# Kernel optimization log

Hardware: AMD Instinct MI355X
Metric: run time of the kernel (lower is better)

Reference implementation:

```python
import jax, jax.numpy as jnp
import numpy as np
from jax import lax

V, D, B, L, T, H, C = 100000, 128, 512, 20, 20, 32, 33
N, E = B * L, B * (L - 1)
SCALE = 12.0

def _l2n(x, eps=1e-12):
    return x / (jnp.linalg.norm(x, axis=-1, keepdims=True) + eps)

def setup_inputs():
    key = jax.random.key(0)
    ks = jax.random.split(key, 30)
    stdv = 1.0 / np.sqrt(D)
    u = lambda k, s: jax.random.uniform(k, s, jnp.float32, -stdv, stdv)
    params = dict(
        emb=u(ks[0], (V, D)),
        W1=u(ks[1], (D, D)), W2=u(ks[2], (D, D)),
        gru_wih=u(ks[3], (3 * D, 2 * D)), gru_whh=u(ks[4], (3 * D, D)),
        gru_bih=u(ks[5], (3 * D,)), gru_bhh=u(ks[6], (3 * D,)),
        fcu_w=u(ks[7], (D, D)), fcv_w=u(ks[8], (D, D)), fcv_b=u(ks[9], (D,)),
        fce_w=u(ks[10], (D,)), fcsr_w=u(ks[11], (D, 2 * D)),
        red_w=u(ks[12], (H, D)), red_b=u(ks[13], (H,)),
        rec_w=u(ks[14], (D, H)), rec_b=u(ks[15], (D,)),
        cde_w1=u(ks[16], (128, H)), cde_b1=u(ks[17], (128,)),
        cde_w2=u(ks[18], (C * H, 128)), cde_b2=u(ks[19], (C * H,)),
        init_w=u(ks[20], (H, C)), init_b=u(ks[21], (H,)),
    )
    nodes = jnp.arange(N).reshape(B, L)  # B session graphs, L nodes each
    params.update(
        w=jax.random.uniform(ks[22], (E,), jnp.float32, 0.1, 1.0),
        times=jnp.cumsum(jax.random.uniform(ks[23], (B, T), jnp.float32, 0.05, 1.0), axis=1),
        iid=jax.random.randint(ks[24], (N,), 0, V),
        src=nodes[:, :-1].reshape(-1),
        dst=nodes[:, 1:].reshape(-1),
        seg_ids=jnp.repeat(jnp.arange(B), L),
        last_nodes=nodes[:, -1],
        embeds_ids=jax.random.randint(ks[25], (B, T), 0, V),
    )
    return params

def reference(emb, W1, W2, gru_wih, gru_whh, gru_bih, gru_bhh, fcu_w, fcv_w, fcv_b,
              fce_w, fcsr_w, red_w, red_b, rec_w, rec_b, cde_w1, cde_b1, cde_w2,
              cde_b2, init_w, init_b, w, times, iid, src, dst, seg_ids, last_nodes,
              embeds_ids):
    feat = _l2n(emb[iid])  # [N,D]
    # --- SRGNN layer: edge-weighted mean message passing (both directions) + GRUCell ---
    def wmean(s, d):
        msum = jax.ops.segment_sum(feat[s] * w[:, None], d, num_segments=N)
        wsum = jax.ops.segment_sum(w, d, num_segments=N)[:, None]
        return jnp.where(wsum > 0, msum / jnp.where(wsum == 0, 1.0, wsum), 0.0)
    hn = jnp.concatenate([wmean(src, dst) @ W1.T, wmean(dst, src) @ W2.T], axis=1)
    gi = hn @ gru_wih.T + gru_bih
    gh = feat @ gru_whh.T + gru_bhh
    i_r, i_z, i_n = jnp.split(gi, 3, axis=1)
    h_r, h_z, h_n = jnp.split(gh, 3, axis=1)
    r = jax.nn.sigmoid(i_r + h_r)
    zg = jax.nn.sigmoid(i_z + h_z)
    ng = jnp.tanh(i_n + r * h_n)
    out = (1.0 - zg) * ng + zg * feat  # NOTE: computed but unused downstream, exactly as original
    # --- neural CDE over the session item sequence (linear interp knots at t=0..T-1, RK4 per knot) ---
    fode = _l2n(emb[embeds_ids] @ red_w.T + red_b)          # [B,T,H]
    X = jnp.concatenate([times[..., None], fode], axis=-1)  # [B,T,C]
    z0 = X[:, 0] @ init_w.T + init_b                        # [B,H]
    def fz(zt):
        h1 = jax.nn.relu(zt @ cde_w1.T + cde_b1)
        return jnp.tanh(h1 @ cde_w2.T + cde_b2).reshape(B, H, C)
    dX = jnp.swapaxes(X[:, 1:] - X[:, :-1], 0, 1)           # [T-1,B,C] piecewise-constant dX/dt
    def step(zt, dx):
        g = lambda zz: jnp.einsum('bhc,bc->bh', fz(zz), dx)
        k1 = g(zt); k2 = g(zt + 0.5 * k1); k3 = g(zt + 0.5 * k2); k4 = g(zt + k3)
        return zt + (k1 + 2.0 * k2 + 2.0 * k3 + k4) / 6.0, None
    zT, _ = lax.scan(step, z0, dX)
    time_embeds = zT @ rec_w.T + rec_b                      # [B,D]
    # --- attention readout over graph segments ---
    featn = feat / jnp.linalg.norm(feat, axis=-1, keepdims=True)  # no-eps renorm, as original
    fu = featn @ fcu_w.T
    fv = featn[last_nodes] @ fcv_w.T + fcv_b
    e = jax.nn.sigmoid(fu + fv[seg_ids]) @ fce_w            # [N]
    emax = jax.ops.segment_max(e, seg_ids, num_segments=B)
    ee = jnp.exp(e - emax[seg_ids])
    alpha = ee / jax.ops.segment_sum(ee, seg_ids, num_segments=B)[seg_ids]
    sr_g = jax.ops.segment_sum(featn * alpha[:, None], seg_ids, num_segments=B)
    sr_l = featn[last_nodes]
    sr = _l2n(jnp.concatenate([sr_l, sr_g], axis=1) @ fcsr_w.T + time_embeds)
    logits = sr @ _l2n(emb).T                               # [B,V]
    return jax.nn.log_softmax(SCALE * logits, axis=-1)
```

## Files before the change

kernel.cpp:

```cpp
#include <hip/hip_runtime.h>
#include <cstdint>

#define VN 100000
#define DD 128
#define BB 512
#define LL 20
#define TT 20
#define HH 32
#define CC 33
#define NC (HH*CC)

typedef unsigned int u32;

#define DEV static __device__ __forceinline__

DEV float tanh_fast(float x){ float e=__expf(2.f*x); return 1.f - 2.f/(e+1.f); }

DEV float rdlane(float v, int l){
  return __int_as_float(__builtin_amdgcn_readlane(__float_as_int(v), l));
}

__global__ __launch_bounds__(512, 2) void k_cde(
    const float* __restrict__ emb, const int* __restrict__ eids,
    const float* __restrict__ times,
    const float* __restrict__ red_w, const float* __restrict__ red_b,
    const float* __restrict__ w1, const float* __restrict__ b1,
    const float* __restrict__ w2, const float* __restrict__ b2,
    const float* __restrict__ iw, const float* __restrict__ ib,
    const float* __restrict__ rw, const float* __restrict__ rb,
    float* __restrict__ te){
  __shared__ float s_u[40*DD + 32*129];
  __shared__ float s_X[2*TT*CC];
  __shared__ float s_b1[DD];
  __shared__ float s_h1[2*DD];
  __shared__ float s_z[64], s_zs[64], s_ks[64], s_kp[64], s_kt[64];
  __shared__ float s_dx[2*CC];
  const int t = threadIdx.x;
  const int b0 = blockIdx.x*2;
  const int lane = t & 63;
  const int wv = t >> 6;
  const int h  = t >> 4;
  const int q  = t & 15;
  float* s_er = s_u;
  float* s_rw = s_u + 40*DD;
  float* s_w1 = s_u;

  float w2c[DD];
  {
    const float4* rc4 = (const float4*)(w2 + (size_t)(h*CC+q)*DD);
    #pragma unroll
    for (int j4=0;j4<32;j4++){
      float4 v = rc4[j4];
      w2c[4*j4]=v.x; w2c[4*j4+1]=v.y; w2c[4*j4+2]=v.z; w2c[4*j4+3]=v.w;
    }
  }
  const float b2c = b2[h*CC+q];
  const float b2s = b2[h*CC+16+q];
  const float* rs = w2 + (size_t)(h*CC+16+q)*DD;
  float w2t[8], b2t[4];
  #pragma unroll
  for (int r=0;r<4;r++){
    const float* tr = w2 + (size_t)((4*wv+r)*CC+32)*DD;
    w2t[2*r]   = tr[lane];
    w2t[2*r+1] = tr[64+lane];
    b2t[r]     = b2[(4*wv+r)*CC+32];
  }

  for (int i=t;i<HH*DD;i+=512){ int hh=i>>7, d=i&127; s_rw[hh*129+d]=red_w[i]; }
  if (t<40){ int g=t/TT, tt2=t%TT; s_X[(g*TT+tt2)*CC]=times[(b0+g)*TT+tt2]; }
  for (int pi=t;pi<40*DD;pi+=512){ int r=pi>>7, e=pi&127;
      s_er[pi]=emb[(size_t)eids[b0*TT+r]*DD+e]; }
  __syncthreads();
  for (int task=t; task<40*HH; task+=512){
    int r=task>>5, hh=task&31;
    const float* wr=s_rw+hh*129;
    const float* er=s_er+(size_t)r*DD;
    float acc=red_b[hh];
    #pragma unroll 16
    for(int e=0;e<DD;e++) acc += er[e]*wr[e];
    float ssq=acc*acc;
    #pragma unroll
    for(int o=16;o>0;o>>=1) ssq+=__shfl_xor(ssq,o,32);
    s_X[r*CC+1+hh]=acc/(sqrtf(ssq)+1e-12f);
  }
  __syncthreads();
  for (int i=t;i<DD*HH;i+=512){ int j=i>>5, hh=i&31; s_w1[j*33+hh]=w1[i]; }
  if (t<DD) s_b1[t]=b1[t];
  if (t<64){
    int g=t>>5, hh=t&31;
    float acc=ib[hh];
    const float* x0=s_X+(size_t)(g*TT)*CC;
    #pragma unroll
    for(int c=0;c<CC;c++) acc += x0[c]*iw[hh*CC+c];
    s_z[t]=acc; s_zs[t]=acc;
  }
  __syncthreads();

  const float4* rs4=(const float4*)rs;
  for (int step=0; step<TT-1; step++){
    if (t<2*CC){ int g=t/CC, c=t-g*CC;
      s_dx[t]=s_X[(g*TT+step+1)*CC+c]-s_X[(g*TT+step)*CC+c]; }
    for (int s=0;s<4;s++){
      float4 c0=rs4[0], c1=rs4[1], c2=rs4[2], c3=rs4[3];
      if (t<256){
        const int g=t>>7, j=t&127, gb=(t>>7)*32;
        float zsv=s_zs[lane];
        float acc=s_b1[j];
        const float* wj=s_w1+j*33;
        #pragma unroll
        for(int hh=0;hh<HH;hh++) acc += rdlane(zsv, gb+hh)*wj[hh];
        s_h1[g*DD+j]=fmaxf(acc,0.f);
      }
      __syncthreads();
      {
        float h00=s_h1[lane],    h01=s_h1[64+lane];
        float h10=s_h1[DD+lane], h11=s_h1[DD+64+lane];
        float a00=b2c, a01=b2c, a10=b2s, a11=b2s;
        #pragma unroll
        for (int jc=0;jc<8;jc++){
          float4 n0=c0,n1=c1,n2=c2,n3=c3;
          if (jc<7){ n0=rs4[4*jc+4]; n1=rs4[4*jc+5]; n2=rs4[4*jc+6]; n3=rs4[4*jc+7]; }
          float cf[16]={c0.x,c0.y,c0.z,c0.w, c1.x,c1.y,c1.z,c1.w,
                        c2.x,c2.y,c2.z,c2.w, c3.x,c3.y,c3.z,c3.w};
          #pragma unroll
          for (int jj=0;jj<16;jj++){
            const int j=jc*16+jj;
            float s0 = (j<64)? rdlane(h00,j) : rdlane(h01,j-64);
            float s1 = (j<64)? rdlane(h10,j) : rdlane(h11,j-64);
            a00 += s0*w2c[j]; a01 += s1*w2c[j];
            a10 += s0*cf[jj]; a11 += s1*cf[jj];
          }
          c0=n0; c1=n1; c2=n2; c3=n3;
        }
        float pk0 = tanh_fast(a00)*s_dx[q]    + tanh_fast(a10)*s_dx[16+q];
        float pk1 = tanh_fast(a01)*s_dx[CC+q] + tanh_fast(a11)*s_dx[CC+16+q];
        #pragma unroll
        for (int o=8;o>0;o>>=1){ pk0+=__shfl_xor(pk0,o,16); pk1+=__shfl_xor(pk1,o,16); }
        if (q==0){ s_kp[h]=pk0; s_kp[32+h]=pk1; }
        float p0=w2t[0]*h00+w2t[1]*h01;
        float p1=w2t[0]*h10+w2t[1]*h11;
        float p2=w2t[2]*h00+w2t[3]*h01;
        float p3=w2t[2]*h10+w2t[3]*h11;
        float p4=w2t[4]*h00+w2t[5]*h01;
        float p5=w2t[4]*h10+w2t[5]*h11;
        float p6=w2t[6]*h00+w2t[7]*h01;
        float p7=w2t[6]*h10+w2t[7]*h11;
        #pragma unroll
        for (int o=1;o<64;o<<=1){
          p0+=__shfl_xor(p0,o,64); p1+=__shfl_xor(p1,o,64);
          p2+=__shfl_xor(p2,o,64); p3+=__shfl_xor(p3,o,64);
          p4+=__shfl_xor(p4,o,64); p5+=__shfl_xor(p5,o,64);
          p6+=__shfl_xor(p6,o,64); p7+=__shfl_xor(p7,o,64);
        }
        if (lane==0){
          float dt0=s_dx[32], dt1=s_dx[CC+32];
          s_kt[4*wv+0]   =tanh_fast(p0+b2t[0])*dt0;
          s_kt[32+4*wv+0]=tanh_fast(p1+b2t[0])*dt1;
          s_kt[4*wv+1]   =tanh_fast(p2+b2t[1])*dt0;
          s_kt[32+4*wv+1]=tanh_fast(p3+b2t[1])*dt1;
          s_kt[4*wv+2]   =tanh_fast(p4+b2t[2])*dt0;
          s_kt[32+4*wv+2]=tanh_fast(p5+b2t[2])*dt1;
          s_kt[4*wv+3]   =tanh_fast(p6+b2t[3])*dt0;
          s_kt[32+4*wv+3]=tanh_fast(p7+b2t[3])*dt1;
        }
      }
      __syncthreads();
      if (t<64){
        float k=s_kp[t]+s_kt[t];
        float zv=s_z[t];
        if(s==0){ s_ks[t]=k;        s_zs[t]=zv+0.5f*k; }
        else if(s==1){ s_ks[t]+=2.f*k; s_zs[t]=zv+0.5f*k; }
        else if(s==2){ s_ks[t]+=2.f*k; s_zs[t]=zv+k; }
        else { float zn=zv+(s_ks[t]+k)*(1.f/6.f); s_z[t]=zn; s_zs[t]=zn; }
      }
      __syncthreads();
    }
  }
  if (t<256){
    const int g=t>>7, d=t&127;
    float acc=rb[d];
    const float* zz=s_z+g*HH;
    const float4* rv=(const float4*)(rw + (size_t)d*HH);
    #pragma unroll
    for(int jj=0;jj<8;jj++){
      float4 vv=rv[jj];
      acc += zz[4*jj]*vv.x + zz[4*jj+1]*vv.y + zz[4*jj+2]*vv.z + zz[4*jj+3]*vv.w;
    }
    te[(size_t)(b0+g)*DD+d]=acc;
  }
}

__global__ __launch_bounds__(128) void k_attn(
    const float* __restrict__ emb, const int* __restrict__ iid,
    const int* __restrict__ last_nodes,
    const float* __restrict__ fcu_w, const float* __restrict__ fcv_w,
    const float* __restrict__ fcv_b, const float* __restrict__ fce_w,
    const float* __restrict__ fcsr_w,
    const float* __restrict__ te, float* __restrict__ sr){
  __shared__ float s_fn[LL*DD];
  __shared__ float s_inv[LL];
  __shared__ float s_e[LL], s_alpha[LL], s_red[2], s_sg[DD], s_fl[DD];
  const int t=threadIdx.x, b=blockIdx.x;
  for(int p=t;p<LL*DD;p+=128){
    int r=p>>7, e=p&127;
    s_fn[p]=emb[(size_t)iid[b*LL+r]*DD+e];
  }
  __syncthreads();
  { int w=t>>6, lane=t&63;
    for(int r=w;r<LL;r+=2){
      float a=s_fn[r*DD+lane], c=s_fn[r*DD+lane+64];
      float s=a*a+c*c;
      #pragma unroll
      for(int o=32;o>0;o>>=1) s+=__shfl_xor(s,o,64);
      if(lane==0) s_inv[r]=1.f/sqrtf(s);
    }
  }
  __syncthreads();
  for(int p=t;p<LL*DD;p+=128) s_fn[p]*=s_inv[p>>7];
  __syncthreads();
  int lr=last_nodes[b]-b*LL; if(lr<0||lr>=LL) lr=LL-1;
  s_fl[t]=s_fn[lr*DD+t];
  __syncthreads();
  float fv;
  {
    float acc=fcv_b[t];
    const float* wv=fcv_w + t*DD;
    #pragma unroll 8
    for(int j=0;j<DD;j++) acc += s_fl[j]*wv[j];
    fv=acc;
  }
  const float fce=fce_w[t];
  const float* wu=fcu_w + t*DD;
  for(int n=0;n<LL;n++){
    float fu=0.f;
    #pragma unroll 8
    for(int j=0;j<DD;j++) fu += s_fn[n*DD+j]*wu[j];
    float sv = fce/(1.f+__expf(-(fu+fv)));
    #pragma unroll
    for(int o=32;o>0;o>>=1) sv += __shfl_xor(sv,o,64);
    if((t&63)==0) s_red[t>>6]=sv;
    __syncthreads();
    if(t==0) s_e[n]=s_red[0]+s_red[1];
    __syncthreads();
  }
  if(t<64){
    float ev=(t<LL)? s_e[t] : -1e30f;
    float m=ev;
    #pragma unroll
    for(int o=32;o>0;o>>=1) m=fmaxf(m,__shfl_xor(m,o,64));
    float ex=(t<LL)? __expf(ev-m):0.f;
    float ssum=ex;
    #pragma unroll
    for(int o=32;o>0;o>>=1) ssum+=__shfl_xor(ssum,o,64);
    if(t<LL) s_alpha[t]=ex/ssum;
  }
  __syncthreads();
  float sg=0.f;
  for(int n=0;n<LL;n++) sg += s_alpha[n]*s_fn[n*DD+t];
  s_sg[t]=sg;
  __syncthreads();
  float pre=te[(size_t)b*DD+t];
  const float* wsr=fcsr_w + t*2*DD;
  #pragma unroll 8
  for(int j=0;j<DD;j++) pre += s_fl[j]*wsr[j];
  #pragma unroll 8
  for(int j=0;j<DD;j++) pre += s_sg[j]*wsr[DD+j];
  float ss=pre*pre;
  #pragma unroll
  for(int o=32;o>0;o>>=1) ss+=__shfl_xor(ss,o,64);
  if((t&63)==0) s_red[t>>6]=ss;
  __syncthreads();
  float tot=s_red[0]+s_red[1];
  sr[(size_t)b*DD+t]=pre/(sqrtf(tot)+1e-12f);
}

__global__ __launch_bounds__(256, 2) void k_logits(
    const float* __restrict__ emb, const float* __restrict__ srr,
    float* __restrict__ out){
  const int v=blockIdx.x*256+threadIdx.x;
  if(v>=VN) return;
  const int bstart=blockIdx.y*256;
  float er[DD];
  {
    const float4* ev=(const float4*)emb + (size_t)v*32;
    #pragma unroll
    for(int j=0;j<32;j++){
      float4 u=ev[j];
      er[j*4+0]=u.x; er[j*4+1]=u.y; er[j*4+2]=u.z; er[j*4+3]=u.w;
    }
  }
  float nrm=0.f;
  #pragma unroll
  for(int d=0;d<DD;d++) nrm += er[d]*er[d];
  const float rn=12.f/(sqrtf(nrm)+1e-12f);
  for(int b=bstart;b<bstart+256;b++){
    const float* s=srr+(size_t)b*DD;
    float acc=0.f;
    #pragma unroll
    for(int d=0;d<DD;d++) acc += er[d]*s[d];
    out[(size_t)b*VN+v]=acc*rn;
  }
}

__global__ __launch_bounds__(256) void k_lse(const float* __restrict__ out,
                                             float* __restrict__ lse){
  const int b=blockIdx.x, t=threadIdx.x;
  const float4* rp=(const float4*)(out + (size_t)b*VN);
  float m=-1e30f, s=0.f;
  for(int i=t;i<VN/4;i+=256){
    float4 x=rp[i];
    float mx=fmaxf(fmaxf(x.x,x.y),fmaxf(x.z,x.w));
    if(mx>m){ s=s*__expf(m-mx); m=mx; }
    s += __expf(x.x-m)+__expf(x.y-m)+__expf(x.z-m)+__expf(x.w-m);
  }
  __shared__ float sm[256], ssb[256];
  sm[t]=m; ssb[t]=s;
  __syncthreads();
  for(int o=128;o>0;o>>=1){
    if(t<o){
      float m1=sm[t], m2=sm[t+o], s1=ssb[t], s2=ssb[t+o];
      float mm=fmaxf(m1,m2);
      sm[t]=mm; ssb[t]=s1*__expf(m1-mm)+s2*__expf(m2-mm);
    }
    __syncthreads();
  }
  if(t==0) lse[b]=sm[0]+logf(ssb[0]);
}

__global__ __launch_bounds__(256) void k_sub(float* __restrict__ out,
                                             const float* __restrict__ lse){
  const size_t i=(size_t)blockIdx.x*256+threadIdx.x;
  const int b=(int)((i*4)/VN);
  const float l=lse[b];
  float4* p=(float4*)out;
  float4 x=p[i];
  x.x-=l; x.y-=l; x.z-=l; x.w-=l;
  p[i]=x;
}

extern "C" void kernel_launch(void* const* d_in, const int* in_sizes, int n_in,
                              void* d_out, int out_size, void* d_ws, size_t ws_size,
                              hipStream_t stream){
  const float* emb    = (const float*)d_in[0];
  const float* fcu_w  = (const float*)d_in[7];
  const float* fcv_w  = (const float*)d_in[8];
  const float* fcv_b  = (const float*)d_in[9];
  const float* fce_w  = (const float*)d_in[10];
  const float* fcsr_w = (const float*)d_in[11];
  const float* red_w  = (const float*)d_in[12];
  const float* red_b  = (const float*)d_in[13];
  const float* rec_w  = (const float*)d_in[14];
  const float* rec_b  = (const float*)d_in[15];
  const float* cde_w1 = (const float*)d_in[16];
  const float* cde_b1 = (const float*)d_in[17];
  const float* cde_w2 = (const float*)d_in[18];
  const float* cde_b2 = (const float*)d_in[19];
  const float* init_w = (const float*)d_in[20];
  const float* init_b = (const float*)d_in[21];
  const float* times  = (const float*)d_in[23];
  const int* iid    = (const int*)d_in[24];
  const int* last_nodes = (const int*)d_in[28];
  const int* embeds_ids = (const int*)d_in[29];
  float* out = (float*)d_out;

  float* ws  = (float*)d_ws;
  float* te  = ws;
  float* sr  = te + (size_t)BB*DD;
  float* lse = sr + (size_t)BB*DD;

  k_cde   <<<BB/2, 512, 0, stream>>>(emb, embeds_ids, times, red_w, red_b,
                                     cde_w1, cde_b1, cde_w2, cde_b2,
                                     init_w, init_b, rec_w, rec_b, te);
  k_attn  <<<BB, 128, 0, stream>>>(emb, iid, last_nodes, fcu_w, fcv_w, fcv_b,
                                   fce_w, fcsr_w, te, sr);
  k_logits<<<dim3((VN+255)/256, 2), 256, 0, stream>>>(emb, sr, out);
  k_lse   <<<BB, 256, 0, stream>>>(out, lse);
  k_sub   <<<(int)(((size_t)BB*VN/4+255)/256), 256, 0, stream>>>(out, lse);
}
```

Before: 3.304 ms.

## Batch four sessions per CDE block and tile logits over staged session vectors

```diff
diff --git a/kernel.cpp b/kernel.cpp
--- a/kernel.cpp
+++ b/kernel.cpp
@@ -9,6 +9,7 @@
 #define HH 32
 #define CC 33
 #define NC (HH*CC)
+#define GG 4
 
 typedef unsigned int u32;
 
@@ -20,7 +21,7 @@
   return __int_as_float(__builtin_amdgcn_readlane(__float_as_int(v), l));
 }
 
-__global__ __launch_bounds__(512, 2) void k_cde(
+__global__ __launch_bounds__(512) void k_cde(
     const float* __restrict__ emb, const int* __restrict__ eids,
     const float* __restrict__ times,
     const float* __restrict__ red_w, const float* __restrict__ red_b,
@@ -29,49 +30,29 @@
     const float* __restrict__ iw, const float* __restrict__ ib,
     const float* __restrict__ rw, const float* __restrict__ rb,
     float* __restrict__ te){
-  __shared__ float s_u[40*DD + 32*129];
-  __shared__ float s_X[2*TT*CC];
+  __shared__ float s_u[GG*TT*DD + 32*129];
+  __shared__ float s_X[GG*TT*CC];
   __shared__ float s_b1[DD];
-  __shared__ float s_h1[2*DD];
-  __shared__ float s_z[64], s_zs[64], s_ks[64], s_kp[64], s_kt[64];
-  __shared__ float s_dx[2*CC];
+  __shared__ float s_b2[NC];
+  __shared__ float s_h1[GG*DD];
+  __shared__ float s_z[GG*HH], s_zs[GG*HH], s_ks[GG*HH], s_kp[GG*HH], s_kt[GG*HH];
+  __shared__ float s_dx[GG*CC];
   const int t = threadIdx.x;
-  const int b0 = blockIdx.x*2;
+  const int b0 = blockIdx.x*GG;
   const int lane = t & 63;
   const int wv = t >> 6;
   const int h  = t >> 4;
   const int q  = t & 15;
   float* s_er = s_u;
-  float* s_rw = s_u + 40*DD;
+  float* s_rw = s_u + GG*TT*DD;
   float* s_w1 = s_u;
 
-  float w2c[DD];
-  {
-    const float4* rc4 = (const float4*)(w2 + (size_t)(h*CC+q)*DD);
-    #pragma unroll
-    for (int j4=0;j4<32;j4++){
-      float4 v = rc4[j4];
-      w2c[4*j4]=v.x; w2c[4*j4+1]=v.y; w2c[4*j4+2]=v.z; w2c[4*j4+3]=v.w;
-    }
-  }
-  const float b2c = b2[h*CC+q];
-  const float b2s = b2[h*CC+16+q];
-  const float* rs = w2 + (size_t)(h*CC+16+q)*DD;
-  float w2t[8], b2t[4];
-  #pragma unroll
-  for (int r=0;r<4;r++){
-    const float* tr = w2 + (size_t)((4*wv+r)*CC+32)*DD;
-    w2t[2*r]   = tr[lane];
-    w2t[2*r+1] = tr[64+lane];
-    b2t[r]     = b2[(4*wv+r)*CC+32];
-  }
-
   for (int i=t;i<HH*DD;i+=512){ int hh=i>>7, d=i&127; s_rw[hh*129+d]=red_w[i]; }
-  if (t<40){ int g=t/TT, tt2=t%TT; s_X[(g*TT+tt2)*CC]=times[(b0+g)*TT+tt2]; }
-  for (int pi=t;pi<40*DD;pi+=512){ int r=pi>>7, e=pi&127;
+  if (t<GG*TT){ int g=t/TT, tt2=t%TT; s_X[(g*TT+tt2)*CC]=times[(b0+g)*TT+tt2]; }
+  for (int pi=t;pi<GG*TT*DD;pi+=512){ int r=pi>>7, e=pi&127;
       s_er[pi]=emb[(size_t)eids[b0*TT+r]*DD+e]; }
   __syncthreads();
-  for (int task=t; task<40*HH; task+=512){
+  for (int task=t; task<GG*TT*HH; task+=512){
     int r=task>>5, hh=task&31;
     const float* wr=s_rw+hh*129;
     const float* er=s_er+(size_t)r*DD;
@@ -84,9 +65,11 @@
     s_X[r*CC+1+hh]=acc/(sqrtf(ssq)+1e-12f);
   }
   __syncthreads();
+
   for (int i=t;i<DD*HH;i+=512){ int j=i>>5, hh=i&31; s_w1[j*33+hh]=w1[i]; }
   if (t<DD) s_b1[t]=b1[t];
-  if (t<64){
+  for (int i=t;i<NC;i+=512) s_b2[i]=b2[i];
+  if (t<GG*HH){
     int g=t>>5, hh=t&31;
     float acc=ib[hh];
     const float* x0=s_X+(size_t)(g*TT)*CC;
@@ -96,76 +79,112 @@
   }
   __syncthreads();
 
-  const float4* rs4=(const float4*)rs;
+  const float4* r1 = (const float4*)(w2 + (size_t)(h*CC+q)*DD);
+  const float4* r2 = (const float4*)(w2 + (size_t)(h*CC+16+q)*DD);
+  const float* tr0 = w2 + (size_t)((4*wv+0)*CC+32)*DD;
+  const float* tr1 = w2 + (size_t)((4*wv+1)*CC+32)*DD;
+  const float* tr2 = w2 + (size_t)((4*wv+2)*CC+32)*DD;
+  const float* tr3 = w2 + (size_t)((4*wv+3)*CC+32)*DD;
+  const float bA = s_b2[h*CC+q];
+  const float bB = s_b2[h*CC+16+q];
+
   for (int step=0; step<TT-1; step++){
-    if (t<2*CC){ int g=t/CC, c=t-g*CC;
+    if (t<GG*CC){ int g=t/CC, c=t-g*CC;
       s_dx[t]=s_X[(g*TT+step+1)*CC+c]-s_X[(g*TT+step)*CC+c]; }
     for (int s=0;s<4;s++){
-      float4 c0=rs4[0], c1=rs4[1], c2=rs4[2], c3=rs4[3];
-      if (t<256){
-        const int g=t>>7, j=t&127, gb=(t>>7)*32;
-        float zsv=s_zs[lane];
+      {
+        const int g=t>>7, j=t&127;
+        float zsv=s_zs[g*HH + (lane&31)];
         float acc=s_b1[j];
         const float* wj=s_w1+j*33;
         #pragma unroll
-        for(int hh=0;hh<HH;hh++) acc += rdlane(zsv, gb+hh)*wj[hh];
+        for(int hh=0;hh<HH;hh++) acc += rdlane(zsv, hh)*wj[hh];
         s_h1[g*DD+j]=fmaxf(acc,0.f);
       }
       __syncthreads();
       {
-        float h00=s_h1[lane],    h01=s_h1[64+lane];
-        float h10=s_h1[DD+lane], h11=s_h1[DD+64+lane];
-        float a00=b2c, a01=b2c, a10=b2s, a11=b2s;
+        const float hA0=s_h1[lane],      hB0=s_h1[64+lane];
+        const float hA1=s_h1[DD+lane],   hB1=s_h1[DD+64+lane];
+        const float hA2=s_h1[2*DD+lane], hB2=s_h1[2*DD+64+lane];
+        const float hA3=s_h1[3*DD+lane], hB3=s_h1[3*DD+64+lane];
+        const float wt0=tr0[lane], wt1=tr0[64+lane];
+        const float wt2=tr1[lane], wt3=tr1[64+lane];
+        const float wt4=tr2[lane], wt5=tr2[64+lane];
+        const float wt6=tr3[lane], wt7=tr3[64+lane];
+        float aA0=0.f,aA1=0.f,aA2=0.f,aA3=0.f;
+        float aB0=0.f,aB1=0.f,aB2=0.f,aB3=0.f;
         #pragma unroll
-        for (int jc=0;jc<8;jc++){
-          float4 n0=c0,n1=c1,n2=c2,n3=c3;
-          if (jc<7){ n0=rs4[4*jc+4]; n1=rs4[4*jc+5]; n2=rs4[4*jc+6]; n3=rs4[4*jc+7]; }
-          float cf[16]={c0.x,c0.y,c0.z,c0.w, c1.x,c1.y,c1.z,c1.w,
-                        c2.x,c2.y,c2.z,c2.w, c3.x,c3.y,c3.z,c3.w};
+        for (int j4=0;j4<32;j4++){
+          const float4 wa=r1[j4];
+          const float4 wb=r2[j4];
           #pragma unroll
-          for (int jj=0;jj<16;jj++){
-            const int j=jc*16+jj;
-            float s0 = (j<64)? rdlane(h00,j) : rdlane(h01,j-64);
-            float s1 = (j<64)? rdlane(h10,j) : rdlane(h11,j-64);
-            a00 += s0*w2c[j]; a01 += s1*w2c[j];
-            a10 += s0*cf[jj]; a11 += s1*cf[jj];
+          for (int e=0;e<4;e++){
+            const int jj=4*j4+e;
+            const float wea = e==0?wa.x : e==1?wa.y : e==2?wa.z : wa.w;
+            const float web = e==0?wb.x : e==1?wb.y : e==2?wb.z : wb.w;
+            const float s0 = (jj<64)? rdlane(hA0,jj) : rdlane(hB0,jj-64);
+            const float s1 = (jj<64)? rdlane(hA1,jj) : rdlane(hB1,jj-64);
+            const float s2 = (jj<64)? rdlane(hA2,jj) : rdlane(hB2,jj-64);
+            const float s3 = (jj<64)? rdlane(hA3,jj) : rdlane(hB3,jj-64);
+            aA0 += s0*wea; aB0 += s0*web;
+            aA1 += s1*wea; aB1 += s1*web;
+            aA2 += s2*wea; aB2 += s2*web;
+            aA3 += s3*wea; aB3 += s3*web;
           }
-          c0=n0; c1=n1; c2=n2; c3=n3;
         }
-        float pk0 = tanh_fast(a00)*s_dx[q]    + tanh_fast(a10)*s_dx[16+q];
-        float pk1 = tanh_fast(a01)*s_dx[CC+q] + tanh_fast(a11)*s_dx[CC+16+q];
+        float k0 = tanh_fast(aA0+bA)*s_dx[q]      + tanh_fast(aB0+bB)*s_dx[16+q];
+        float k1 = tanh_fast(aA1+bA)*s_dx[CC+q]   + tanh_fast(aB1+bB)*s_dx[CC+16+q];
+        float k2 = tanh_fast(aA2+bA)*s_dx[2*CC+q] + tanh_fast(aB2+bB)*s_dx[2*CC+16+q];
+        float k3 = tanh_fast(aA3+bA)*s_dx[3*CC+q] + tanh_fast(aB3+bB)*s_dx[3*CC+16+q];
         #pragma unroll
-        for (int o=8;o>0;o>>=1){ pk0+=__shfl_xor(pk0,o,16); pk1+=__shfl_xor(pk1,o,16); }
-        if (q==0){ s_kp[h]=pk0; s_kp[32+h]=pk1; }
-        float p0=w2t[0]*h00+w2t[1]*h01;
-        float p1=w2t[0]*h10+w2t[1]*h11;
-        float p2=w2t[2]*h00+w2t[3]*h01;
-        float p3=w2t[2]*h10+w2t[3]*h11;
-        float p4=w2t[4]*h00+w2t[5]*h01;
-        float p5=w2t[4]*h10+w2t[5]*h11;
-        float p6=w2t[6]*h00+w2t[7]*h01;
-        float p7=w2t[6]*h10+w2t[7]*h11;
+        for (int o=8;o>0;o>>=1){
+          k0+=__shfl_xor(k0,o,16); k1+=__shfl_xor(k1,o,16);
+          k2+=__shfl_xor(k2,o,16); k3+=__shfl_xor(k3,o,16);
+        }
+        if (q==0){ s_kp[h]=k0; s_kp[HH+h]=k1; s_kp[2*HH+h]=k2; s_kp[3*HH+h]=k3; }
+        float p00=wt0*hA0+wt1*hB0, p01=wt0*hA1+wt1*hB1,
+              p02=wt0*hA2+wt1*hB2, p03=wt0*hA3+wt1*hB3;
+        float p10=wt2*hA0+wt3*hB0, p11=wt2*hA1+wt3*hB1,
+              p12=wt2*hA2+wt3*hB2, p13=wt2*hA3+wt3*hB3;
+        float p20=wt4*hA0+wt5*hB0, p21=wt4*hA1+wt5*hB1,
+              p22=wt4*hA2+wt5*hB2, p23=wt4*hA3+wt5*hB3;
+        float p30=wt6*hA0+wt7*hB0, p31=wt6*hA1+wt7*hB1,
+              p32=wt6*hA2+wt7*hB2, p33=wt6*hA3+wt7*hB3;
         #pragma unroll
         for (int o=1;o<64;o<<=1){
-          p0+=__shfl_xor(p0,o,64); p1+=__shfl_xor(p1,o,64);
-          p2+=__shfl_xor(p2,o,64); p3+=__shfl_xor(p3,o,64);
-          p4+=__shfl_xor(p4,o,64); p5+=__shfl_xor(p5,o,64);
-          p6+=__shfl_xor(p6,o,64); p7+=__shfl_xor(p7,o,64);
+          p00+=__shfl_xor(p00,o,64); p01+=__shfl_xor(p01,o,64);
+          p02+=__shfl_xor(p02,o,64); p03+=__shfl_xor(p03,o,64);
+          p10+=__shfl_xor(p10,o,64); p11+=__shfl_xor(p11,o,64);
+          p12+=__shfl_xor(p12,o,64); p13+=__shfl_xor(p13,o,64);
+          p20+=__shfl_xor(p20,o,64); p21+=__shfl_xor(p21,o,64);
+          p22+=__shfl_xor(p22,o,64); p23+=__shfl_xor(p23,o,64);
+          p30+=__shfl_xor(p30,o,64); p31+=__shfl_xor(p31,o,64);
+          p32+=__shfl_xor(p32,o,64); p33+=__shfl_xor(p33,o,64);
         }
         if (lane==0){
-          float dt0=s_dx[32], dt1=s_dx[CC+32];
-          s_kt[4*wv+0]   =tanh_fast(p0+b2t[0])*dt0;
-          s_kt[32+4*wv+0]=tanh_fast(p1+b2t[0])*dt1;
-          s_kt[4*wv+1]   =tanh_fast(p2+b2t[1])*dt0;
-          s_kt[32+4*wv+1]=tanh_fast(p3+b2t[1])*dt1;
-          s_kt[4*wv+2]   =tanh_fast(p4+b2t[2])*dt0;
-          s_kt[32+4*wv+2]=tanh_fast(p5+b2t[2])*dt1;
-          s_kt[4*wv+3]   =tanh_fast(p6+b2t[3])*dt0;
-          s_kt[32+4*wv+3]=tanh_fast(p7+b2t[3])*dt1;
+          const float btl0=s_b2[(4*wv+0)*CC+32], btl1=s_b2[(4*wv+1)*CC+32];
+          const float btl2=s_b2[(4*wv+2)*CC+32], btl3=s_b2[(4*wv+3)*CC+32];
+          const float d0=s_dx[32], d1=s_dx[CC+32], d2=s_dx[2*CC+32], d3=s_dx[3*CC+32];
+          s_kt[     4*wv+0]=tanh_fast(p00+btl0)*d0;
+          s_kt[HH  +4*wv+0]=tanh_fast(p01+btl0)*d1;
+          s_kt[2*HH+4*wv+0]=tanh_fast(p02+btl0)*d2;
+          s_kt[3*HH+4*wv+0]=tanh_fast(p03+btl0)*d3;
+          s_kt[     4*wv+1]=tanh_fast(p10+btl1)*d0;
+          s_kt[HH  +4*wv+1]=tanh_fast(p11+btl1)*d1;
+          s_kt[2*HH+4*wv+1]=tanh_fast(p12+btl1)*d2;
+          s_kt[3*HH+4*wv+1]=tanh_fast(p13+btl1)*d3;
+          s_kt[     4*wv+2]=tanh_fast(p20+btl2)*d0;
+          s_kt[HH  +4*wv+2]=tanh_fast(p21+btl2)*d1;
+          s_kt[2*HH+4*wv+2]=tanh_fast(p22+btl2)*d2;
+          s_kt[3*HH+4*wv+2]=tanh_fast(p23+btl2)*d3;
+          s_kt[     4*wv+3]=tanh_fast(p30+btl3)*d0;
+          s_kt[HH  +4*wv+3]=tanh_fast(p31+btl3)*d1;
+          s_kt[2*HH+4*wv+3]=tanh_fast(p32+btl3)*d2;
+          s_kt[3*HH+4*wv+3]=tanh_fast(p33+btl3)*d3;
         }
       }
       __syncthreads();
-      if (t<64){
+      if (t<GG*HH){
         float k=s_kp[t]+s_kt[t];
         float zv=s_z[t];
         if(s==0){ s_ks[t]=k;        s_zs[t]=zv+0.5f*k; }
@@ -176,7 +195,7 @@
       __syncthreads();
     }
   }
-  if (t<256){
+  {
     const int g=t>>7, d=t&127;
     float acc=rb[d];
     const float* zz=s_z+g*HH;
@@ -224,9 +243,9 @@
   float fv;
   {
     float acc=fcv_b[t];
-    const float* wv=fcv_w + t*DD;
+    const float* wvv=fcv_w + t*DD;
     #pragma unroll 8
-    for(int j=0;j<DD;j++) acc += s_fl[j]*wv[j];
+    for(int j=0;j<DD;j++) acc += s_fl[j]*wvv[j];
     fv=acc;
   }
   const float fce=fce_w[t];
@@ -274,32 +293,36 @@
   sr[(size_t)b*DD+t]=pre/(sqrtf(tot)+1e-12f);
 }
 
-__global__ __launch_bounds__(256, 2) void k_logits(
+#define BT 64
+__global__ __launch_bounds__(256) void k_logits(
     const float* __restrict__ emb, const float* __restrict__ srr,
     float* __restrict__ out){
-  const int v=blockIdx.x*256+threadIdx.x;
-  if(v>=VN) return;
-  const int bstart=blockIdx.y*256;
-  float er[DD];
-  {
-    const float4* ev=(const float4*)emb + (size_t)v*32;
-    #pragma unroll
-    for(int j=0;j<32;j++){
-      float4 u=ev[j];
-      er[j*4+0]=u.x; er[j*4+1]=u.y; er[j*4+2]=u.z; er[j*4+3]=u.w;
+  __shared__ float s_sr[BT*DD];
+  const int tdx=threadIdx.x;
+  const int btile=blockIdx.y;
+  for (int i=tdx;i<BT*DD;i+=256) s_sr[i]=srr[(size_t)btile*BT*DD+i];
+  __syncthreads();
+  const int v=blockIdx.x*256+tdx;
+  if (v>=VN) return;
+  const float4* ev=(const float4*)(emb+(size_t)v*DD);
+  const float4* sr4=(const float4*)s_sr;
+  float acc[BT];
+  #pragma unroll
+  for (int b=0;b<BT;b++) acc[b]=0.f;
+  float nrm=0.f;
+  for (int j4=0;j4<32;j4++){
+    const float4 e4=ev[j4];
+    nrm += e4.x*e4.x+e4.y*e4.y+e4.z*e4.z+e4.w*e4.w;
+    #pragma unroll
+    for (int b=0;b<BT;b++){
+      const float4 s4=sr4[b*32+j4];
+      acc[b] += e4.x*s4.x+e4.y*s4.y+e4.z*s4.z+e4.w*s4.w;
     }
   }
-  float nrm=0.f;
+  const float rn=12.f/(sqrtf(nrm)+1e-12f);
   #pragma unroll
-  for(int d=0;d<DD;d++) nrm += er[d]*er[d];
-  const float rn=12.f/(sqrtf(nrm)+1e-12f);
-  for(int b=bstart;b<bstart+256;b++){
-    const float* s=srr+(size_t)b*DD;
-    float acc=0.f;
-    #pragma unroll
-    for(int d=0;d<DD;d++) acc += er[d]*s[d];
-    out[(size_t)b*VN+v]=acc*rn;
-  }
+  for (int b=0;b<BT;b++)
+    out[(size_t)(btile*BT+b)*VN+v]=acc[b]*rn;
 }
 
 __global__ __launch_bounds__(256) void k_lse(const float* __restrict__ out,
@@ -368,12 +391,12 @@
   float* sr  = te + (size_t)BB*DD;
   float* lse = sr + (size_t)BB*DD;
 
-  k_cde   <<<BB/2, 512, 0, stream>>>(emb, embeds_ids, times, red_w, red_b,
-                                     cde_w1, cde_b1, cde_w2, cde_b2,
-                                     init_w, init_b, rec_w, rec_b, te);
+  k_cde   <<<BB/GG, 512, 0, stream>>>(emb, embeds_ids, times, red_w, red_b,
+                                      cde_w1, cde_b1, cde_w2, cde_b2,
+                                      init_w, init_b, rec_w, rec_b, te);
   k_attn  <<<BB, 128, 0, stream>>>(emb, iid, last_nodes, fcu_w, fcv_w, fcv_b,
                                    fce_w, fcsr_w, te, sr);
-  k_logits<<<dim3((VN+255)/256, 2), 256, 0, stream>>>(emb, sr, out);
+  k_logits<<<dim3((VN+255)/256, BB/BT), 256, 0, stream>>>(emb, sr, out);
   k_lse   <<<BB, 256, 0, stream>>>(out, lse);
   k_sub   <<<(int)(((size_t)BB*VN/4+255)/256), 256, 0, stream>>>(out, lse);
 }
```

After: 3.334 ms. About the same (+0.9%).
